# Performance work log

Hardware: AMD Instinct MI355X
Metric: run time of the kernel (lower is better)

The kernel has to match this reference:

```python
import jax, jax.numpy as jnp
import numpy as np

KERNELS = (4, 4, 8, 8, 8, 16, 16)
HEADS = (4, 4, 8, 8, 8, 16, 16)
PATCH = 2
EPS = 1e-5


def _layer_norm(x, w, b):
    mu = jnp.mean(x, axis=-1, keepdims=True)
    var = jnp.mean(jnp.square(x - mu), axis=-1, keepdims=True)
    return (x - mu) * jax.lax.rsqrt(var + EPS) * w + b


def _sliding_kernel_attention(x, w_qkv, k, heads):
    # x: (B, H, W, C) channels-last. Unfold -> per-window attention over the
    # k*k pixels (token dim = C) -> overlap-add fold (stride 1).
    B, H, W, C = x.shape
    Lh, Lw = H - k + 1, W - k + 1
    scale = (C // heads) ** -0.5
    ih = jnp.arange(Lh)[:, None] + jnp.arange(k)[None, :]   # (Lh, k)
    iw = jnp.arange(Lw)[:, None] + jnp.arange(k)[None, :]   # (Lw, k)
    pat = x[:, ih][:, :, :, iw]                             # (B, Lh, k, Lw, k, C)
    tok = pat.transpose(0, 1, 3, 2, 4, 5).reshape(B, Lh * Lw, k * k, C)
    qkv = jnp.einsum('blnc,dc->blnd', tok, w_qkv)           # (B, L, k*k, 3C)
    q, kk, v = jnp.split(qkv, 3, axis=-1)
    attn = jax.nn.softmax(jnp.einsum('blqc,blkc->blqk', q, kk) * scale, axis=-1)
    o = jnp.einsum('blqk,blkc->blqc', attn, v)              # (B, L, k*k, C)
    o = o.reshape(B, Lh, Lw, k, k, C).transpose(0, 1, 3, 2, 4, 5)  # (B,Lh,k,Lw,k,C)
    # overlap-add fold back to (B, H, W, C); duplicate indices accumulate
    return jnp.zeros_like(x).at[:, ih[:, :, None, None], iw[None, None, :, :], :].add(o)


def _block(x, ln1_w, ln1_b, w_qkv, ln2_w, ln2_b, w1, b1, w2, b2, k, heads):
    x = x + _sliding_kernel_attention(_layer_norm(x, ln1_w, ln1_b), w_qkv, k, heads)
    h = _layer_norm(x, ln2_w, ln2_b)
    h = jax.nn.gelu(h @ w1.T + b1, approximate=False)
    return x + (h @ w2.T + b2)


def _forward(x, patch_w, patch_b, row_emb, col_emb, cls_tok, ln1_w, ln1_b, qkv_w,
             ln2_w, ln2_b, mlp_w1, mlp_b1, mlp_w2, mlp_b2, cls_w, cls_b):
    # patch embed: conv k=stride=PATCH; output laid out channels-last (B, G, G, C)
    h = jax.lax.conv_general_dilated(
        x, patch_w, (PATCH, PATCH), 'VALID',
        dimension_numbers=('NCHW', 'OIHW', 'NHWC')) + patch_b
    B, G, _, C = h.shape
    # 2D positional embedding: row half + col half concatenated on channels
    pos = jnp.concatenate([
        jnp.broadcast_to(row_emb[:, None, :], (G, G, C // 2)),
        jnp.broadcast_to(col_emb[None, :, :], (G, G, C // 2))], axis=-1)
    h = h + pos
    # cls token: one extra row prepended along H (torch cat on dim=2)
    cls = jnp.broadcast_to(cls_tok, (B, 1, G, C))
    h = jnp.concatenate([cls, h], axis=1)                   # (B, G+1, G, C)
    for i in range(7):
        h = _block(h, ln1_w[i], ln1_b[i], qkv_w[i], ln2_w[i], ln2_b[i],
                   mlp_w1[i], mlp_b1[i], mlp_w2[i], mlp_b2[i],
                   KERNELS[i], HEADS[i])
    return h[:, 0, 0, :] @ cls_w.T + cls_b                  # (B, num_classes)


def setup_inputs() -> dict:
    key = jax.random.key(0)
    ks = jax.random.split(key, 8)
    B, C, G, NCLS, NB = 16, 256, 16, 1000, 7
    s = 0.02
    return {
        'x': jax.random.normal(ks[0], (B, 3, 32, 32), jnp.float32),
        'patch_w': jax.random.normal(ks[1], (C, 3, PATCH, PATCH), jnp.float32) * s,
        'patch_b': jnp.zeros((C,), jnp.float32),
        'row_emb': jax.random.normal(ks[2], (G, C // 2), jnp.float32) * s,
        'col_emb': jax.random.normal(ks[3], (G, C // 2), jnp.float32) * s,
        'cls_tok': jnp.zeros((C,), jnp.float32),
        'ln1_w': jnp.ones((NB, C), jnp.float32),
        'ln1_b': jnp.zeros((NB, C), jnp.float32),
        'qkv_w': jax.random.normal(ks[4], (NB, 3 * C, C), jnp.float32) * s,
        'ln2_w': jnp.ones((NB, C), jnp.float32),
        'ln2_b': jnp.zeros((NB, C), jnp.float32),
        'mlp_w1': jax.random.normal(ks[5], (NB, 2 * C, C), jnp.float32) * s,
        'mlp_b1': jnp.zeros((NB, 2 * C), jnp.float32),
        'mlp_w2': jax.random.normal(ks[6], (NB, C, 2 * C), jnp.float32) * s,
        'mlp_b2': jnp.zeros((NB, C), jnp.float32),
        'cls_w': jax.random.normal(ks[7], (NCLS, C), jnp.float32) * s,
        'cls_b': jnp.zeros((NCLS,), jnp.float32),
    }


def reference(x, patch_w, patch_b, row_emb, col_emb, cls_tok, ln1_w, ln1_b, qkv_w,
              ln2_w, ln2_b, mlp_w1, mlp_b1, mlp_w2, mlp_b2, cls_w, cls_b):
    return _forward(x, patch_w, patch_b, row_emb, col_emb, cls_tok, ln1_w, ln1_b,
                    qkv_w, ln2_w, ln2_b, mlp_w1, mlp_b1, mlp_w2, mlp_b2, cls_w, cls_b)
```

## Files before the change

kernel.cpp:

```cpp
#include <hip/hip_runtime.h>
#include <cmath>

#define NPIX 4352
#define C_DIM 256

typedef unsigned short ushort_t;
typedef unsigned int uint_t;
typedef float f32x4 __attribute__((ext_vector_type(4)));
typedef __bf16 bfx8 __attribute__((ext_vector_type(8)));

__device__ __forceinline__ ushort_t f2bf(float f) {
    uint_t u = __float_as_uint(f);
    u = (u + 0x7FFFu + ((u >> 16) & 1u)) >> 16;
    return (ushort_t)u;
}
__device__ __forceinline__ float bf2f(ushort_t b) {
    return __uint_as_float(((uint_t)b) << 16);
}
__device__ __forceinline__ float gelu_f(float v) {
    return 0.5f * v * (1.0f + erff(v * 0.70710678118654752f));
}

__global__ __launch_bounds__(256) void conv3_bf16(
    const float* __restrict__ a, ushort_t* __restrict__ oa, int na,
    const float* __restrict__ b, ushort_t* __restrict__ ob, int nb,
    const float* __restrict__ c, ushort_t* __restrict__ oc, int nc)
{
    int ntot = na + nb + nc;
    for (int i = blockIdx.x * 256 + threadIdx.x; i < ntot; i += gridDim.x * 256) {
        if (i < na)            oa[i] = f2bf(a[i]);
        else if (i < na + nb)  ob[i - na] = f2bf(b[i - na]);
        else                   oc[i - na - nb] = f2bf(c[i - na - nb]);
    }
}

__global__ __launch_bounds__(256) void patch_embed_ln(
    const float* __restrict__ x, const float* __restrict__ pw,
    const float* __restrict__ pb, const float* __restrict__ row_emb,
    const float* __restrict__ col_emb, const float* __restrict__ cls_tok,
    const float* __restrict__ lw, const float* __restrict__ lb,
    float* __restrict__ out, ushort_t* __restrict__ lnout)
{
    __shared__ float red[8];
    int p = blockIdx.x;
    int c = threadIdx.x;
    int b = p / 272;
    int rem = p - b * 272;
    int y = rem >> 4;
    int xw = rem & 15;
    float v;
    if (y == 0) {
        v = cls_tok[c];
    } else {
        int gr = y - 1, gc = xw;
        const float* xb = x + (size_t)b * 3 * 1024;
        const float* wc = pw + (size_t)c * 12;
        float acc = pb[c];
        #pragma unroll
        for (int ci = 0; ci < 3; ci++)
            #pragma unroll
            for (int ph = 0; ph < 2; ph++)
                #pragma unroll
                for (int pq = 0; pq < 2; pq++)
                    acc += xb[ci * 1024 + (2 * gr + ph) * 32 + (2 * gc + pq)]
                         * wc[(ci * 2 + ph) * 2 + pq];
        acc += (c < 128) ? row_emb[gr * 128 + c] : col_emb[gc * 128 + (c - 128)];
        v = acc;
    }
    out[(size_t)p * C_DIM + c] = v;
    float s = v;
    s += __shfl_down(s, 32); s += __shfl_down(s, 16); s += __shfl_down(s, 8);
    s += __shfl_down(s, 4);  s += __shfl_down(s, 2);  s += __shfl_down(s, 1);
    if ((c & 63) == 0) red[c >> 6] = s;
    __syncthreads();
    float mu = (red[0] + red[1] + red[2] + red[3]) * (1.0f / 256.0f);
    float d = v - mu;
    float s2 = d * d;
    s2 += __shfl_down(s2, 32); s2 += __shfl_down(s2, 16); s2 += __shfl_down(s2, 8);
    s2 += __shfl_down(s2, 4);  s2 += __shfl_down(s2, 2);  s2 += __shfl_down(s2, 1);
    if ((c & 63) == 0) red[4 + (c >> 6)] = s2;
    __syncthreads();
    float var = (red[4] + red[5] + red[6] + red[7]) * (1.0f / 256.0f);
    lnout[(size_t)p * C_DIM + c] = f2bf(d * rsqrtf(var + 1e-5f) * lw[c] + lb[c]);
}

__global__ __launch_bounds__(256) void layernorm_k(
    const float* __restrict__ in, const float* __restrict__ w,
    const float* __restrict__ b, ushort_t* __restrict__ out)
{
    __shared__ float red[8];
    int r = blockIdx.x, c = threadIdx.x;
    float v = in[(size_t)r * C_DIM + c];
    float s = v;
    s += __shfl_down(s, 32); s += __shfl_down(s, 16); s += __shfl_down(s, 8);
    s += __shfl_down(s, 4);  s += __shfl_down(s, 2);  s += __shfl_down(s, 1);
    if ((c & 63) == 0) red[c >> 6] = s;
    __syncthreads();
    float mu = (red[0] + red[1] + red[2] + red[3]) * (1.0f / 256.0f);
    float d = v - mu;
    float s2 = d * d;
    s2 += __shfl_down(s2, 32); s2 += __shfl_down(s2, 16); s2 += __shfl_down(s2, 8);
    s2 += __shfl_down(s2, 4);  s2 += __shfl_down(s2, 2);  s2 += __shfl_down(s2, 1);
    if ((c & 63) == 0) red[4 + (c >> 6)] = s2;
    __syncthreads();
    float var = (red[4] + red[5] + red[6] + red[7]) * (1.0f / 256.0f);
    out[(size_t)r * C_DIM + c] = f2bf(d * rsqrtf(var + 1e-5f) * w[c] + b[c]);
}

template <int BM, int BN, int MODE>
__global__ __launch_bounds__(256) void gemm_v2(
    const ushort_t* __restrict__ A, const ushort_t* __restrict__ B,
    const float* __restrict__ bias, const float* __restrict__ res,
    void* __restrict__ outp, ushort_t* __restrict__ vT, int K, int ldo)
{
    constexpr int MI = BM / 32, NJ = BN / 32;
    constexpr int AG = BM * 4, BG = BN * 4;
    constexpr int AU = AG / 256, BU = BG / 256;
    constexpr int HALF = (BM + BN) * 32;
    constexpr int STAGE_E = 2 * HALF;
    constexpr int BOUNCE_E = BM * (BN + 8);
    constexpr int SMEM_E = (STAGE_E > BOUNCE_E) ? STAGE_E : BOUNCE_E;
    __shared__ ushort_t sm[SMEM_E];

    int m0 = blockIdx.x * BM, n0 = blockIdx.y * BN;
    int t = threadIdx.x, lane = t & 63, wv = t >> 6;
    int l15 = lane & 15, lg = lane >> 4;
    int wr = wv >> 1, wc = wv & 1;

    const int nt = K / 32;
    f32x4 acc[MI][NJ] = {};
    uint4 ra[AU], rb[BU];

    #pragma unroll
    for (int u = 0; u < AU; u++) {
        int g = t + u * 256, row = g >> 2, p = g & 3;
        int ps = p ^ ((row >> 1) & 3);
        ra[u] = *(const uint4*)(A + (size_t)(m0 + row) * K + ps * 8);
    }
    #pragma unroll
    for (int u = 0; u < BU; u++) {
        int g = t + u * 256, col = g >> 2, p = g & 3;
        int ps = p ^ ((col >> 1) & 3);
        rb[u] = *(const uint4*)(B + (size_t)(n0 + col) * K + ps * 8);
    }
    #pragma unroll
    for (int u = 0; u < AU; u++) *(uint4*)(sm + (t + u * 256) * 8) = ra[u];
    #pragma unroll
    for (int u = 0; u < BU; u++) *(uint4*)(sm + BM * 32 + (t + u * 256) * 8) = rb[u];
    __syncthreads();

    for (int ks = 0; ks < nt; ks++) {
        int coff = (ks & 1) * HALF, noff = ((ks & 1) ^ 1) * HALF;
        if (ks + 1 < nt) {
            int k1 = (ks + 1) * 32;
            #pragma unroll
            for (int u = 0; u < AU; u++) {
                int g = t + u * 256, row = g >> 2, p = g & 3;
                int ps = p ^ ((row >> 1) & 3);
                ra[u] = *(const uint4*)(A + (size_t)(m0 + row) * K + k1 + ps * 8);
            }
            #pragma unroll
            for (int u = 0; u < BU; u++) {
                int g = t + u * 256, col = g >> 2, p = g & 3;
                int ps = p ^ ((col >> 1) & 3);
                rb[u] = *(const uint4*)(B + (size_t)(n0 + col) * K + k1 + ps * 8);
            }
        }
        bfx8 af[MI], bf[NJ];
        #pragma unroll
        for (int i = 0; i < MI; i++) {
            int row = wr * (BM / 2) + i * 16 + l15;
            af[i] = *(const bfx8*)(sm + coff + row * 32 + ((lg ^ ((row >> 1) & 3)) << 3));
        }
        #pragma unroll
        for (int j = 0; j < NJ; j++) {
            int col = wc * (BN / 2) + j * 16 + l15;
            bf[j] = *(const bfx8*)(sm + coff + BM * 32 + col * 32 + ((lg ^ ((col >> 1) & 3)) << 3));
        }
        #pragma unroll
        for (int i = 0; i < MI; i++)
            #pragma unroll
            for (int j = 0; j < NJ; j++)
                acc[i][j] = __builtin_amdgcn_mfma_f32_16x16x32_bf16(af[i], bf[j], acc[i][j], 0, 0, 0);
        if (ks + 1 < nt) {
            #pragma unroll
            for (int u = 0; u < AU; u++) *(uint4*)(sm + noff + (t + u * 256) * 8) = ra[u];
            #pragma unroll
            for (int u = 0; u < BU; u++) *(uint4*)(sm + noff + BM * 32 + (t + u * 256) * 8) = rb[u];
        }
        __syncthreads();
    }

    if (MODE == 0 && n0 >= 512) {
        #pragma unroll
        for (int i = 0; i < MI; i++) {
            int mb = m0 + wr * (BM / 2) + i * 16 + lg * 4;
            #pragma unroll
            for (int j = 0; j < NJ; j++) {
                int nv = n0 - 512 + wc * (BN / 2) + j * 16 + l15;
                ushort4 pk;
                pk.x = f2bf(acc[i][j][0]); pk.y = f2bf(acc[i][j][1]);
                pk.z = f2bf(acc[i][j][2]); pk.w = f2bf(acc[i][j][3]);
                *(ushort4*)&vT[(size_t)nv * NPIX + mb] = pk;
            }
        }
        return;
    }
    if (MODE == 3) {
        float* o = (float*)outp;
        #pragma unroll
        for (int i = 0; i < MI; i++) {
            #pragma unroll
            for (int j = 0; j < NJ; j++) {
                int col = n0 + wc * (BN / 2) + j * 16 + l15;
                float bz = bias[col];
                #pragma unroll
                for (int r = 0; r < 4; r++) {
                    int row = m0 + wr * (BM / 2) + i * 16 + lg * 4 + r;
                    o[(size_t)row * ldo + col] = acc[i][j][r] + bz + res[(size_t)row * ldo + col];
                }
            }
        }
        return;
    }
    __syncthreads();
    #pragma unroll
    for (int i = 0; i < MI; i++) {
        #pragma unroll
        for (int j = 0; j < NJ; j++) {
            int cl = wc * (BN / 2) + j * 16 + l15;
            float bz = (MODE == 2) ? bias[n0 + cl] : 0.0f;
            #pragma unroll
            for (int r = 0; r < 4; r++) {
                int rl = wr * (BM / 2) + i * 16 + lg * 4 + r;
                float v = acc[i][j][r];
                if (MODE == 2) v = gelu_f(v + bz);
                sm[rl * (BN + 8) + cl] = f2bf(v);
            }
        }
    }
    __syncthreads();
    ushort_t* ob = (ushort_t*)outp;
    #pragma unroll
    for (int e = 0; e < BM * BN; e += 2048) {
        int idx = e + t * 8;
        int rl = idx / BN, cl = idx % BN;
        uint4 v = *(const uint4*)(sm + rl * (BN + 8) + cl);
        *(uint4*)&ob[(size_t)(m0 + rl) * ldo + n0 + cl] = v;
    }
}

__device__ __forceinline__ uint2 ld_u4_align(const uint_t* drow, int e0) {
    int d0 = e0 >> 1;
    if (!(e0 & 1)) return make_uint2(drow[d0], drow[d0 + 1]);
    uint_t a = drow[d0], b = drow[d0 + 1], c = drow[d0 + 2];
    return make_uint2((a >> 16) | (b << 16), (b >> 16) | (c << 16));
}
__device__ __forceinline__ uint4 ld_u8_align(const uint_t* drow, int e0) {
    int d0 = e0 >> 1;
    if (!(e0 & 1)) return make_uint4(drow[d0], drow[d0 + 1], drow[d0 + 2], drow[d0 + 3]);
    uint_t a = drow[d0], b = drow[d0 + 1], c = drow[d0 + 2], d = drow[d0 + 3], e = drow[d0 + 4];
    return make_uint4((a >> 16) | (b << 16), (b >> 16) | (c << 16),
                      (c >> 16) | (d << 16), (d >> 16) | (e << 16));
}

template <int KK>
__global__ __launch_bounds__(256) void attn_v2(
    const ushort_t* __restrict__ qk, const ushort_t* __restrict__ vT,
    ushort_t* __restrict__ obuf, int w0, int nW, float scale)
{
    constexpr int T = KK * KK;
    constexpr int Lh = 18 - KK, Lw = 17 - KK, L = Lh * Lw;
    constexpr int NCH  = (KK == 16) ? 4 : 1;
    constexpr int NF   = (KK == 4) ? 1 : 4;
    constexpr int NJ   = 8;
    constexpr int PSTR = (KK == 4) ? 40 : 72;
    constexpr int KROWS = (KK == 4) ? 32 : 64;
    constexpr int VROWS = (KK == 4) ? 256 : 128;
    constexpr int PVKT = (KK == 4) ? 1 : 2;
    constexpr int EOFF = (KK == 4) ? 2048 : 4096;
    constexpr int ESTR = (KK == 4) ? 128 : 134;

    __shared__ ushort_t Klds[KROWS * 256];
    __shared__ ushort_t Vlds[VROWS * 64];
    __shared__ ushort_t Plds[4][16 * PSTR];

    int t = threadIdx.x, lane = t & 63, wv = t >> 6;
    int l15 = lane & 15, lg = lane >> 4;

    int wrel, qbase, chalf, wloc;
    if (KK == 4)      { wrel = blockIdx.x * 2 + (wv & 1); wloc = wv & 1; chalf = wv >> 1; qbase = 0; }
    else if (KK == 8) { wrel = blockIdx.x >> 1; wloc = 0; chalf = blockIdx.x & 1; qbase = wv * 16; }
    else              { wrel = blockIdx.x >> 3; wloc = 0; chalf = blockIdx.x & 1;
                        qbase = ((blockIdx.x >> 1) & 3) * 64 + wv * 16; }
    if (wrel >= nW) wrel = nW - 1;

    int pbs[2];
    #pragma unroll
    for (int w = 0; w < 2; w++) {
        int wi = (KK == 4) ? blockIdx.x * 2 + w : wrel;
        if (wi >= nW) wi = nW - 1;
        wi += w0;
        int b = wi / L, lrem = wi % L;
        pbs[w] = b * 272 + (lrem / Lw) * 16 + (lrem % Lw);
    }

    int qtok = qbase + l15;
    int qpix;
    if (KK == 4)      qpix = pbs[wloc] + ((qtok >> 2) << 4) + (qtok & 3);
    else if (KK == 8) qpix = pbs[0] + ((qtok >> 3) << 4) + (qtok & 7);
    else              qpix = pbs[0] + qtok;
    bfx8 qf[8];
    #pragma unroll
    for (int cs = 0; cs < 8; cs++)
        qf[cs] = *(const bfx8*)(qk + (size_t)qpix * 512 + cs * 32 + lg * 8);

    f32x4 o[NJ] = {};
    float mold[4] = {-1e30f, -1e30f, -1e30f, -1e30f};
    float lsum[4] = {0.f, 0.f, 0.f, 0.f};

    for (int ch = 0; ch < NCH; ch++) {
        int c0 = ch * 64;
        if (ch > 0) __syncthreads();
        for (int g = t; g < KROWS * 32; g += 256) {
            int row = g >> 5, cg = g & 31;
            int pix;
            if (KK == 4)      pix = pbs[row >> 4] + (((row & 15) >> 2) << 4) + (row & 3);
            else if (KK == 8) pix = pbs[0] + ((row >> 3) << 4) + (row & 7);
            else              pix = pbs[0] + c0 + row;
            uint4 v = *(const uint4*)(qk + (size_t)pix * 512 + 256 + cg * 8);
            *(uint4*)(Klds + row * 256 + ((cg ^ (row & 7)) << 3)) = v;
        }
        for (int g = t; g < VROWS * 8; g += 256) {
            int cr = g >> 3, c16 = g & 7;
            int cglob = (KK == 4) ? cr : chalf * 128 + cr;
            const uint_t* drow = (const uint_t*)(vT + (size_t)cglob * NPIX);
            uint4 v;
            if (KK == 4) {
                int w = c16 >> 2, sub = c16 & 3;
                if (sub < 2) {
                    int pix0 = pbs[w] + (sub << 5);
                    uint2 a  = ld_u4_align(drow, pix0);
                    uint2 b2 = ld_u4_align(drow, pix0 + 16);
                    v = make_uint4(a.x, a.y, b2.x, b2.y);
                } else v = make_uint4(0, 0, 0, 0);
            } else if (KK == 8) {
                v = ld_u8_align(drow, pbs[0] + (c16 << 4));
            } else {
                v = *(const uint4*)(vT + (size_t)cglob * NPIX + pbs[0] + c0 + (c16 << 3));
            }
            *(uint4*)(Vlds + cr * 64 + ((c16 ^ (cr & 7)) << 3)) = v;
        }
        __syncthreads();
        f32x4 s[NF];
        #pragma unroll
        for (int j = 0; j < NF; j++) s[j] = f32x4{0.f, 0.f, 0.f, 0.f};
        #pragma unroll
        for (int cs = 0; cs < 8; cs++) {
            #pragma unroll
            for (int j = 0; j < NF; j++) {
                int krow = (KK == 4) ? (wloc << 4) + l15 : (j << 4) + l15;
                bfx8 kf = *(const bfx8*)(Klds + krow * 256 + ((((cs << 2) + lg) ^ (krow & 7)) << 3));
                s[j] = __builtin_amdgcn_mfma_f32_16x16x32_bf16(qf[cs], kf, s[j], 0, 0, 0);
            }
        }
        float alpha[4];
        float p[NF][4];
        #pragma unroll
        for (int r = 0; r < 4; r++) {
            float mx = s[0][r];
            #pragma unroll
            for (int j = 1; j < NF; j++) mx = fmaxf(mx, s[j][r]);
            mx = fmaxf(mx, __shfl_xor(mx, 1));
            mx = fmaxf(mx, __shfl_xor(mx, 2));
            mx = fmaxf(mx, __shfl_xor(mx, 4));
            mx = fmaxf(mx, __shfl_xor(mx, 8));
            float mnew = fmaxf(mold[r], mx);
            alpha[r] = __expf(scale * (mold[r] - mnew));
            float ps = 0.f;
            #pragma unroll
            for (int j = 0; j < NF; j++) {
                p[j][r] = __expf(scale * (s[j][r] - mnew));
                ps += p[j][r];
            }
            ps += __shfl_xor(ps, 1);
            ps += __shfl_xor(ps, 2);
            ps += __shfl_xor(ps, 4);
            ps += __shfl_xor(ps, 8);
            lsum[r] = lsum[r] * alpha[r] + ps;
            mold[r] = mnew;
        }
        if (NCH > 1) {
            #pragma unroll
            for (int j = 0; j < NJ; j++) {
                o[j][0] *= alpha[0]; o[j][1] *= alpha[1];
                o[j][2] *= alpha[2]; o[j][3] *= alpha[3];
            }
        }
        ushort_t* Pw = Plds[wv];
        #pragma unroll
        for (int j = 0; j < NF; j++)
            #pragma unroll
            for (int r = 0; r < 4; r++)
                Pw[(lg * 4 + r) * PSTR + (j << 4) + l15] = f2bf(p[j][r]);
        if (KK == 4) {
            #pragma unroll
            for (int r = 0; r < 4; r++)
                Pw[(lg * 4 + r) * PSTR + 16 + l15] = 0;
        }
        asm volatile("s_waitcnt lgkmcnt(0)" ::: "memory");
        __builtin_amdgcn_sched_barrier(0);
        #pragma unroll
        for (int kt = 0; kt < PVKT; kt++) {
            bfx8 pf = *(const bfx8*)(Pw + l15 * PSTR + (kt << 5) + (lg << 3));
            #pragma unroll
            for (int j = 0; j < NJ; j++) {
                int cr = (KK == 4) ? chalf * 128 + (j << 4) + l15 : (j << 4) + l15;
                int c16 = ((KK == 4) ? (wloc << 2) + lg : (kt << 2) + lg) ^ (cr & 7);
                bfx8 vf = *(const bfx8*)(Vlds + cr * 64 + (c16 << 3));
                o[j] = __builtin_amdgcn_mfma_f32_16x16x32_bf16(pf, vf, o[j], 0, 0, 0);
            }
        }
    }
    asm volatile("s_waitcnt lgkmcnt(0)" ::: "memory");
    __syncthreads();
    float inv[4];
    #pragma unroll
    for (int r = 0; r < 4; r++) inv[r] = 1.0f / lsum[r];
    ushort_t* Ep = Klds + wv * EOFF;
    #pragma unroll
    for (int j = 0; j < NJ; j++)
        #pragma unroll
        for (int r = 0; r < 4; r++)
            Ep[(lg * 4 + r) * ESTR + (j << 4) + l15] = f2bf(o[j][r] * inv[r]);
    asm volatile("s_waitcnt lgkmcnt(0)" ::: "memory");
    __builtin_amdgcn_sched_barrier(0);
    size_t gb = ((size_t)wrel * T + qbase) * C_DIM + chalf * 128;
    #pragma unroll
    for (int i = 0; i < 4; i++) {
        int off = i * 512 + lane * 8;
        int row = off >> 7, col = off & 127;
        uint4 v = *(const uint4*)(Ep + row * ESTR + col);
        *(uint4*)(obuf + gb + (size_t)row * C_DIM + col) = v;
    }
}

__global__ __launch_bounds__(256) void fold_ln(
    const ushort_t* __restrict__ obuf, const float* __restrict__ xin,
    float* __restrict__ y, const float* __restrict__ lw,
    const float* __restrict__ lb, ushort_t* __restrict__ lnout, int do_ln,
    int k, int Lh, int Lw, int w0, int w1)
{
    __shared__ float red[8];
    int p = blockIdx.x;
    int c = threadIdx.x;
    int b = p / 272;
    int rem = p - b * 272;
    int yy = rem >> 4, xx = rem & 15;
    int L = Lh * Lw;
    int T = k * k;
    float acc = xin ? xin[(size_t)p * C_DIM + c] : y[(size_t)p * C_DIM + c];
    int lh0 = max(0, yy - k + 1), lh1 = min(Lh - 1, yy);
    int lw0 = max(0, xx - k + 1), lw1 = min(Lw - 1, xx);
    for (int lh = lh0; lh <= lh1; lh++) {
        for (int lw = lw0; lw <= lw1; lw++) {
            int widx = b * L + lh * Lw + lw;
            if (widx < w0 || widx >= w1) continue;
            int n = (yy - lh) * k + (xx - lw);
            acc += bf2f(obuf[((size_t)(widx - w0) * T + n) * C_DIM + c]);
        }
    }
    y[(size_t)p * C_DIM + c] = acc;
    if (!do_ln) return;
    float s = acc;
    s += __shfl_down(s, 32); s += __shfl_down(s, 16); s += __shfl_down(s, 8);
    s += __shfl_down(s, 4);  s += __shfl_down(s, 2);  s += __shfl_down(s, 1);
    if ((c & 63) == 0) red[c >> 6] = s;
    __syncthreads();
    float mu = (red[0] + red[1] + red[2] + red[3]) * (1.0f / 256.0f);
    float d = acc - mu;
    float s2 = d * d;
    s2 += __shfl_down(s2, 32); s2 += __shfl_down(s2, 16); s2 += __shfl_down(s2, 8);
    s2 += __shfl_down(s2, 4);  s2 += __shfl_down(s2, 2);  s2 += __shfl_down(s2, 1);
    if ((c & 63) == 0) red[4 + (c >> 6)] = s2;
    __syncthreads();
    float var = (red[4] + red[5] + red[6] + red[7]) * (1.0f / 256.0f);
    lnout[(size_t)p * C_DIM + c] = f2bf(d * rsqrtf(var + 1e-5f) * lw[c] + lb[c]);
}

__global__ __launch_bounds__(256) void classifier_k(
    const float* __restrict__ h, const float* __restrict__ cw,
    const float* __restrict__ cb, float* __restrict__ out)
{
    __shared__ float hrow[256];
    int b = blockIdx.x;
    int n = blockIdx.y * 256 + threadIdx.x;
    hrow[threadIdx.x] = h[(size_t)b * 272 * C_DIM + threadIdx.x];
    __syncthreads();
    if (n < 1000) {
        float acc = cb[n];
        const float* wr = cw + (size_t)n * C_DIM;
        for (int c = 0; c < 256; c++) acc += hrow[c] * wr[c];
        out[(size_t)b * 1000 + n] = acc;
    }
}

extern "C" void kernel_launch(void* const* d_in, const int* in_sizes, int n_in,
                              void* d_out, int out_size, void* d_ws, size_t ws_size,
                              hipStream_t stream)
{
    const float* x       = (const float*)d_in[0];
    const float* patch_w = (const float*)d_in[1];
    const float* patch_b = (const float*)d_in[2];
    const float* row_emb = (const float*)d_in[3];
    const float* col_emb = (const float*)d_in[4];
    const float* cls_tok = (const float*)d_in[5];
    const float* ln1_w   = (const float*)d_in[6];
    const float* ln1_b   = (const float*)d_in[7];
    const float* qkv_w   = (const float*)d_in[8];
    const float* ln2_w   = (const float*)d_in[9];
    const float* ln2_b   = (const float*)d_in[10];
    const float* mlp_w1  = (const float*)d_in[11];
    const float* mlp_b1  = (const float*)d_in[12];
    const float* mlp_w2  = (const float*)d_in[13];
    const float* mlp_b2  = (const float*)d_in[14];
    const float* cls_w   = (const float*)d_in[15];
    const float* cls_b   = (const float*)d_in[16];
    float* out = (float*)d_out;

    float* xb0  = (float*)d_ws;
    float* xb1  = xb0 + (size_t)NPIX * 256;
    ushort_t* lnb = (ushort_t*)(xb1 + (size_t)NPIX * 256);
    ushort_t* qkb = lnb + (size_t)NPIX * 256;
    ushort_t* vT  = qkb + (size_t)NPIX * 512;
    ushort_t* h1  = vT + (size_t)256 * NPIX;
    ushort_t* wq  = h1 + (size_t)NPIX * 512;
    ushort_t* w1b = wq + (size_t)7 * 768 * 256;
    ushort_t* w2b = w1b + (size_t)7 * 512 * 256;
    ushort_t* obuf = w2b + (size_t)7 * 256 * 512;
    size_t obuf_off_bytes = (size_t)((char*)obuf - (char*)d_ws);
    size_t obuf_cap_e = (ws_size > obuf_off_bytes + 64)
                        ? (ws_size - obuf_off_bytes - 64) / 2 : 0;

    conv3_bf16<<<1024, 256, 0, stream>>>(qkv_w, wq, 7 * 768 * 256,
                                         mlp_w1, w1b, 7 * 512 * 256,
                                         mlp_w2, w2b, 7 * 256 * 512);

    patch_embed_ln<<<NPIX, 256, 0, stream>>>(x, patch_w, patch_b, row_emb,
                                             col_emb, cls_tok, ln1_w, ln1_b,
                                             xb0, lnb);

    const int KS[7] = {4, 4, 8, 8, 8, 16, 16};
    float* xcur = xb0;
    float* ybuf = xb1;

    for (int i = 0; i < 7; i++) {
        int k = KS[i];
        int Lh = 18 - k, Lw = 17 - k, L = Lh * Lw, T = k * k;
        float scale = 1.0f / std::sqrt((float)(256 / k));

        if (i > 0)
            layernorm_k<<<NPIX, 256, 0, stream>>>(xcur, ln1_w + i * 256,
                                                  ln1_b + i * 256, lnb);
        gemm_v2<128, 128, 0><<<dim3(NPIX / 128, 6), 256, 0, stream>>>(
            lnb, wq + (size_t)i * 768 * 256, nullptr, nullptr, qkb, vT, 256, 512);

        int totalW = 16 * L;
        size_t perW = (size_t)T * C_DIM;
        int maxW = (int)((obuf_cap_e / perW) < (size_t)totalW
                         ? (obuf_cap_e / perW) : (size_t)totalW);
        if (maxW < 2) maxW = 2;
        if (k == 4) maxW &= ~1;
        for (int w0 = 0; w0 < totalW; w0 += maxW) {
            int nW = totalW - w0 < maxW ? totalW - w0 : maxW;
            if (k == 4)
                attn_v2<4><<<(nW + 1) / 2, 256, 0, stream>>>(qkb, vT, obuf, w0, nW, scale);
            else if (k == 8)
                attn_v2<8><<<nW * 2, 256, 0, stream>>>(qkb, vT, obuf, w0, nW, scale);
            else
                attn_v2<16><<<nW * 8, 256, 0, stream>>>(qkb, vT, obuf, w0, nW, scale);
            int last = (w0 + nW >= totalW);
            fold_ln<<<NPIX, 256, 0, stream>>>(obuf, (w0 == 0) ? xcur : nullptr,
                                              ybuf, ln2_w + i * 256, ln2_b + i * 256,
                                              lnb, last, k, Lh, Lw, w0, w0 + nW);
        }

        gemm_v2<64, 128, 2><<<dim3(NPIX / 64, 4), 256, 0, stream>>>(
            lnb, w1b + (size_t)i * 512 * 256, mlp_b1 + i * 512, nullptr, h1, nullptr, 256, 512);
        gemm_v2<64, 64, 3><<<dim3(NPIX / 64, 4), 256, 0, stream>>>(
            h1, w2b + (size_t)i * 256 * 512, mlp_b2 + i * 256, ybuf, xcur, nullptr, 512, 256);
    }

    classifier_k<<<dim3(16, 4), 256, 0, stream>>>(xcur, cls_w, cls_b, out);
}
```

Baseline: 763.3 us.

## Add full-window k=8 attention kernel and GEMM-based path for k=16

The k=8 layers get a dedicated attention kernel where one block covers a whole window and all 256 channels, so K and V are staged once instead of split across two channel-half blocks. For k=16, each sequence has only 2x1 windows, so attention becomes three kernels: a batched QK^T GEMM writing fp32 scores, a row softmax, and a PV GEMM. This replaces the chunked online-softmax kernel that launched 8 blocks per window. attn_v2 is reduced to a k=4-only specialization. The cost is extra global round trips for the score and probability buffers and more kernel launches.

```diff
diff --git a/kernel.cpp b/kernel.cpp
--- a/kernel.cpp
+++ b/kernel.cpp
@@ -271,15 +271,13 @@
 {
     constexpr int T = KK * KK;
     constexpr int Lh = 18 - KK, Lw = 17 - KK, L = Lh * Lw;
-    constexpr int NCH  = (KK == 16) ? 4 : 1;
-    constexpr int NF   = (KK == 4) ? 1 : 4;
+    constexpr int NF   = 1;
     constexpr int NJ   = 8;
-    constexpr int PSTR = (KK == 4) ? 40 : 72;
-    constexpr int KROWS = (KK == 4) ? 32 : 64;
-    constexpr int VROWS = (KK == 4) ? 256 : 128;
-    constexpr int PVKT = (KK == 4) ? 1 : 2;
-    constexpr int EOFF = (KK == 4) ? 2048 : 4096;
-    constexpr int ESTR = (KK == 4) ? 128 : 134;
+    constexpr int PSTR = 40;
+    constexpr int KROWS = 32;
+    constexpr int VROWS = 256;
+    constexpr int EOFF = 2048;
+    constexpr int ESTR = 128;
 
     __shared__ ushort_t Klds[KROWS * 256];
     __shared__ ushort_t Vlds[VROWS * 64];
@@ -288,17 +286,14 @@
     int t = threadIdx.x, lane = t & 63, wv = t >> 6;
     int l15 = lane & 15, lg = lane >> 4;
 
-    int wrel, qbase, chalf, wloc;
-    if (KK == 4)      { wrel = blockIdx.x * 2 + (wv & 1); wloc = wv & 1; chalf = wv >> 1; qbase = 0; }
-    else if (KK == 8) { wrel = blockIdx.x >> 1; wloc = 0; chalf = blockIdx.x & 1; qbase = wv * 16; }
-    else              { wrel = blockIdx.x >> 3; wloc = 0; chalf = blockIdx.x & 1;
-                        qbase = ((blockIdx.x >> 1) & 3) * 64 + wv * 16; }
+    int wrel = blockIdx.x * 2 + (wv & 1);
+    int wloc = wv & 1, chalf = wv >> 1, qbase = 0;
     if (wrel >= nW) wrel = nW - 1;
 
     int pbs[2];
     #pragma unroll
     for (int w = 0; w < 2; w++) {
-        int wi = (KK == 4) ? blockIdx.x * 2 + w : wrel;
+        int wi = blockIdx.x * 2 + w;
         if (wi >= nW) wi = nW - 1;
         wi += w0;
         int b = wi / L, lrem = wi % L;
@@ -306,120 +301,77 @@
     }
 
     int qtok = qbase + l15;
-    int qpix;
-    if (KK == 4)      qpix = pbs[wloc] + ((qtok >> 2) << 4) + (qtok & 3);
-    else if (KK == 8) qpix = pbs[0] + ((qtok >> 3) << 4) + (qtok & 7);
-    else              qpix = pbs[0] + qtok;
+    int qpix = pbs[wloc] + ((qtok >> 2) << 4) + (qtok & 3);
     bfx8 qf[8];
     #pragma unroll
     for (int cs = 0; cs < 8; cs++)
         qf[cs] = *(const bfx8*)(qk + (size_t)qpix * 512 + cs * 32 + lg * 8);
 
     f32x4 o[NJ] = {};
-    float mold[4] = {-1e30f, -1e30f, -1e30f, -1e30f};
     float lsum[4] = {0.f, 0.f, 0.f, 0.f};
 
-    for (int ch = 0; ch < NCH; ch++) {
-        int c0 = ch * 64;
-        if (ch > 0) __syncthreads();
-        for (int g = t; g < KROWS * 32; g += 256) {
-            int row = g >> 5, cg = g & 31;
-            int pix;
-            if (KK == 4)      pix = pbs[row >> 4] + (((row & 15) >> 2) << 4) + (row & 3);
-            else if (KK == 8) pix = pbs[0] + ((row >> 3) << 4) + (row & 7);
-            else              pix = pbs[0] + c0 + row;
-            uint4 v = *(const uint4*)(qk + (size_t)pix * 512 + 256 + cg * 8);
-            *(uint4*)(Klds + row * 256 + ((cg ^ (row & 7)) << 3)) = v;
-        }
-        for (int g = t; g < VROWS * 8; g += 256) {
-            int cr = g >> 3, c16 = g & 7;
-            int cglob = (KK == 4) ? cr : chalf * 128 + cr;
-            const uint_t* drow = (const uint_t*)(vT + (size_t)cglob * NPIX);
-            uint4 v;
-            if (KK == 4) {
-                int w = c16 >> 2, sub = c16 & 3;
-                if (sub < 2) {
-                    int pix0 = pbs[w] + (sub << 5);
-                    uint2 a  = ld_u4_align(drow, pix0);
-                    uint2 b2 = ld_u4_align(drow, pix0 + 16);
-                    v = make_uint4(a.x, a.y, b2.x, b2.y);
-                } else v = make_uint4(0, 0, 0, 0);
-            } else if (KK == 8) {
-                v = ld_u8_align(drow, pbs[0] + (c16 << 4));
-            } else {
-                v = *(const uint4*)(vT + (size_t)cglob * NPIX + pbs[0] + c0 + (c16 << 3));
-            }
-            *(uint4*)(Vlds + cr * 64 + ((c16 ^ (cr & 7)) << 3)) = v;
-        }
-        __syncthreads();
-        f32x4 s[NF];
-        #pragma unroll
-        for (int j = 0; j < NF; j++) s[j] = f32x4{0.f, 0.f, 0.f, 0.f};
-        #pragma unroll
-        for (int cs = 0; cs < 8; cs++) {
-            #pragma unroll
-            for (int j = 0; j < NF; j++) {
-                int krow = (KK == 4) ? (wloc << 4) + l15 : (j << 4) + l15;
-                bfx8 kf = *(const bfx8*)(Klds + krow * 256 + ((((cs << 2) + lg) ^ (krow & 7)) << 3));
-                s[j] = __builtin_amdgcn_mfma_f32_16x16x32_bf16(qf[cs], kf, s[j], 0, 0, 0);
-            }
-        }
-        float alpha[4];
-        float p[NF][4];
-        #pragma unroll
-        for (int r = 0; r < 4; r++) {
-            float mx = s[0][r];
-            #pragma unroll
-            for (int j = 1; j < NF; j++) mx = fmaxf(mx, s[j][r]);
-            mx = fmaxf(mx, __shfl_xor(mx, 1));
-            mx = fmaxf(mx, __shfl_xor(mx, 2));
-            mx = fmaxf(mx, __shfl_xor(mx, 4));
-            mx = fmaxf(mx, __shfl_xor(mx, 8));
-            float mnew = fmaxf(mold[r], mx);
-            alpha[r] = __expf(scale * (mold[r] - mnew));
-            float ps = 0.f;
-            #pragma unroll
-            for (int j = 0; j < NF; j++) {
-                p[j][r] = __expf(scale * (s[j][r] - mnew));
-                ps += p[j][r];
-            }
-            ps += __shfl_xor(ps, 1);
-            ps += __shfl_xor(ps, 2);
-            ps += __shfl_xor(ps, 4);
-            ps += __shfl_xor(ps, 8);
-            lsum[r] = lsum[r] * alpha[r] + ps;
-            mold[r] = mnew;
-        }
-        if (NCH > 1) {
-            #pragma unroll
-            for (int j = 0; j < NJ; j++) {
-                o[j][0] *= alpha[0]; o[j][1] *= alpha[1];
-                o[j][2] *= alpha[2]; o[j][3] *= alpha[3];
-            }
-        }
-        ushort_t* Pw = Plds[wv];
-        #pragma unroll
-        for (int j = 0; j < NF; j++)
-            #pragma unroll
-            for (int r = 0; r < 4; r++)
-                Pw[(lg * 4 + r) * PSTR + (j << 4) + l15] = f2bf(p[j][r]);
-        if (KK == 4) {
-            #pragma unroll
-            for (int r = 0; r < 4; r++)
-                Pw[(lg * 4 + r) * PSTR + 16 + l15] = 0;
-        }
-        asm volatile("s_waitcnt lgkmcnt(0)" ::: "memory");
-        __builtin_amdgcn_sched_barrier(0);
-        #pragma unroll
-        for (int kt = 0; kt < PVKT; kt++) {
-            bfx8 pf = *(const bfx8*)(Pw + l15 * PSTR + (kt << 5) + (lg << 3));
-            #pragma unroll
-            for (int j = 0; j < NJ; j++) {
-                int cr = (KK == 4) ? chalf * 128 + (j << 4) + l15 : (j << 4) + l15;
-                int c16 = ((KK == 4) ? (wloc << 2) + lg : (kt << 2) + lg) ^ (cr & 7);
-                bfx8 vf = *(const bfx8*)(Vlds + cr * 64 + (c16 << 3));
-                o[j] = __builtin_amdgcn_mfma_f32_16x16x32_bf16(pf, vf, o[j], 0, 0, 0);
-            }
+    for (int g = t; g < KROWS * 32; g += 256) {
+        int row = g >> 5, cg = g & 31;
+        int pix = pbs[row >> 4] + (((row & 15) >> 2) << 4) + (row & 3);
+        uint4 v = *(const uint4*)(qk + (size_t)pix * 512 + 256 + cg * 8);
+        *(uint4*)(Klds + row * 256 + ((cg ^ (row & 7)) << 3)) = v;
+    }
+    for (int g = t; g < VROWS * 8; g += 256) {
+        int cr = g >> 3, c16 = g & 7;
+        const uint_t* drow = (const uint_t*)(vT + (size_t)cr * NPIX);
+        uint4 v;
+        int w = c16 >> 2, sub = c16 & 3;
+        if (sub < 2) {
+            int pix0 = pbs[w] + (sub << 5);
+            uint2 a  = ld_u4_align(drow, pix0);
+            uint2 b2 = ld_u4_align(drow, pix0 + 16);
+            v = make_uint4(a.x, a.y, b2.x, b2.y);
+        } else v = make_uint4(0, 0, 0, 0);
+        *(uint4*)(Vlds + cr * 64 + ((c16 ^ (cr & 7)) << 3)) = v;
+    }
+    __syncthreads();
+    f32x4 s[NF];
+    #pragma unroll
+    for (int j = 0; j < NF; j++) s[j] = f32x4{0.f, 0.f, 0.f, 0.f};
+    #pragma unroll
+    for (int cs = 0; cs < 8; cs++) {
+        int krow = (wloc << 4) + l15;
+        bfx8 kf = *(const bfx8*)(Klds + krow * 256 + ((((cs << 2) + lg) ^ (krow & 7)) << 3));
+        s[0] = __builtin_amdgcn_mfma_f32_16x16x32_bf16(qf[cs], kf, s[0], 0, 0, 0);
+    }
+    float p[NF][4];
+    #pragma unroll
+    for (int r = 0; r < 4; r++) {
+        float mx = s[0][r];
+        mx = fmaxf(mx, __shfl_xor(mx, 1));
+        mx = fmaxf(mx, __shfl_xor(mx, 2));
+        mx = fmaxf(mx, __shfl_xor(mx, 4));
+        mx = fmaxf(mx, __shfl_xor(mx, 8));
+        float ps = 0.f;
+        p[0][r] = __expf(scale * (s[0][r] - mx));
+        ps += p[0][r];
+        ps += __shfl_xor(ps, 1);
+        ps += __shfl_xor(ps, 2);
+        ps += __shfl_xor(ps, 4);
+        ps += __shfl_xor(ps, 8);
+        lsum[r] = ps;
+    }
+    ushort_t* Pw = Plds[wv];
+    #pragma unroll
+    for (int r = 0; r < 4; r++) {
+        Pw[(lg * 4 + r) * PSTR + l15] = f2bf(p[0][r]);
+        Pw[(lg * 4 + r) * PSTR + 16 + l15] = 0;
+    }
+    asm volatile("s_waitcnt lgkmcnt(0)" ::: "memory");
+    __builtin_amdgcn_sched_barrier(0);
+    {
+        bfx8 pf = *(const bfx8*)(Pw + l15 * PSTR + (lg << 3));
+        #pragma unroll
+        for (int j = 0; j < NJ; j++) {
+            int cr = chalf * 128 + (j << 4) + l15;
+            int c16 = ((wloc << 2) + lg) ^ (cr & 7);
+            bfx8 vf = *(const bfx8*)(Vlds + cr * 64 + (c16 << 3));
+            o[j] = __builtin_amdgcn_mfma_f32_16x16x32_bf16(pf, vf, o[j], 0, 0, 0);
         }
     }
     asm volatile("s_waitcnt lgkmcnt(0)" ::: "memory");
@@ -443,6 +395,249 @@
         uint4 v = *(const uint4*)(Ep + row * ESTR + col);
         *(uint4*)(obuf + gb + (size_t)row * C_DIM + col) = v;
     }
+}
+
+__global__ __launch_bounds__(256) void attn_v3(
+    const ushort_t* __restrict__ qk, const ushort_t* __restrict__ vT,
+    ushort_t* __restrict__ obuf, int w0, float scale)
+{
+    __shared__ ushort_t SH[32768];
+    const int Lw = 9, L = 90;
+    int t = threadIdx.x, lane = t & 63, wv = t >> 6;
+    int l15 = lane & 15, lg = lane >> 4;
+    int wrel = blockIdx.x;
+    int widx = w0 + wrel;
+    int b = widx / L, lrem = widx % L;
+    int pbase = b * 272 + (lrem / Lw) * 16 + (lrem % Lw);
+    int qbase = wv * 16;
+
+    int qtok = qbase + l15;
+    int qpix = pbase + ((qtok >> 3) << 4) + (qtok & 7);
+    bfx8 qf[8];
+    #pragma unroll
+    for (int cs = 0; cs < 8; cs++)
+        qf[cs] = *(const bfx8*)(qk + (size_t)qpix * 512 + cs * 32 + lg * 8);
+
+    for (int g = t; g < 64 * 32; g += 256) {
+        int row = g >> 5, cg = g & 31;
+        int pix = pbase + ((row >> 3) << 4) + (row & 7);
+        uint4 v = *(const uint4*)(qk + (size_t)pix * 512 + 256 + cg * 8);
+        *(uint4*)(SH + row * 256 + ((cg ^ (row & 7)) << 3)) = v;
+    }
+    for (int g = t; g < 256 * 8; g += 256) {
+        int cr = g >> 3, c16 = g & 7;
+        const uint_t* drow = (const uint_t*)(vT + (size_t)cr * NPIX);
+        uint4 v = ld_u8_align(drow, pbase + (c16 << 4));
+        *(uint4*)(SH + 16384 + cr * 64 + ((c16 ^ (cr & 7)) << 3)) = v;
+    }
+    __syncthreads();
+
+    f32x4 s[4];
+    #pragma unroll
+    for (int j = 0; j < 4; j++) s[j] = f32x4{0.f, 0.f, 0.f, 0.f};
+    #pragma unroll
+    for (int cs = 0; cs < 8; cs++) {
+        #pragma unroll
+        for (int j = 0; j < 4; j++) {
+            int krow = (j << 4) + l15;
+            bfx8 kf = *(const bfx8*)(SH + krow * 256 + ((((cs << 2) + lg) ^ (krow & 7)) << 3));
+            s[j] = __builtin_amdgcn_mfma_f32_16x16x32_bf16(qf[cs], kf, s[j], 0, 0, 0);
+        }
+    }
+    float p[4][4], lsum[4];
+    #pragma unroll
+    for (int r = 0; r < 4; r++) {
+        float mx = s[0][r];
+        #pragma unroll
+        for (int j = 1; j < 4; j++) mx = fmaxf(mx, s[j][r]);
+        mx = fmaxf(mx, __shfl_xor(mx, 1));
+        mx = fmaxf(mx, __shfl_xor(mx, 2));
+        mx = fmaxf(mx, __shfl_xor(mx, 4));
+        mx = fmaxf(mx, __shfl_xor(mx, 8));
+        float ps = 0.f;
+        #pragma unroll
+        for (int j = 0; j < 4; j++) {
+            p[j][r] = __expf(scale * (s[j][r] - mx));
+            ps += p[j][r];
+        }
+        ps += __shfl_xor(ps, 1);
+        ps += __shfl_xor(ps, 2);
+        ps += __shfl_xor(ps, 4);
+        ps += __shfl_xor(ps, 8);
+        lsum[r] = ps;
+    }
+    __syncthreads();
+    ushort_t* Pw = SH + wv * 1088;
+    #pragma unroll
+    for (int j = 0; j < 4; j++)
+        #pragma unroll
+        for (int r = 0; r < 4; r++)
+            Pw[(lg * 4 + r) * 68 + (j << 4) + l15] = f2bf(p[j][r]);
+    asm volatile("s_waitcnt lgkmcnt(0)" ::: "memory");
+    __builtin_amdgcn_sched_barrier(0);
+    f32x4 o[16] = {};
+    #pragma unroll
+    for (int kt = 0; kt < 2; kt++) {
+        bfx8 pf = *(const bfx8*)(Pw + l15 * 68 + (kt << 5) + (lg << 3));
+        #pragma unroll
+        for (int j = 0; j < 16; j++) {
+            int cr = (j << 4) + l15;
+            int c16 = ((kt << 2) + lg) ^ (cr & 7);
+            bfx8 vf = *(const bfx8*)(SH + 16384 + cr * 64 + (c16 << 3));
+            o[j] = __builtin_amdgcn_mfma_f32_16x16x32_bf16(pf, vf, o[j], 0, 0, 0);
+        }
+    }
+    asm volatile("s_waitcnt lgkmcnt(0)" ::: "memory");
+    __syncthreads();
+    float inv[4];
+    #pragma unroll
+    for (int r = 0; r < 4; r++) inv[r] = 1.0f / lsum[r];
+    ushort_t* Ep = SH + wv * 4224;
+    #pragma unroll
+    for (int j = 0; j < 16; j++)
+        #pragma unroll
+        for (int r = 0; r < 4; r++)
+            Ep[(lg * 4 + r) * 260 + (j << 4) + l15] = f2bf(o[j][r] * inv[r]);
+    asm volatile("s_waitcnt lgkmcnt(0)" ::: "memory");
+    __builtin_amdgcn_sched_barrier(0);
+    size_t gb = ((size_t)wrel * 64 + qbase) * C_DIM;
+    #pragma unroll
+    for (int i = 0; i < 8; i++) {
+        int off = i * 512 + lane * 8;
+        int row = off >> 8, col = off & 255;
+        uint4 v = *(const uint4*)(Ep + row * 260 + col);
+        *(uint4*)(obuf + gb + off) = v;
+    }
+}
+
+template <int PASS>
+__global__ __launch_bounds__(256) void gemm_seq(
+    const ushort_t* __restrict__ A, const ushort_t* __restrict__ B,
+    const float* __restrict__ linv, void* __restrict__ outp)
+{
+    __shared__ ushort_t sm[8192];
+    int m0 = blockIdx.x * 64, n0 = blockIdx.y * 64;
+    int seq = blockIdx.z;
+    int pbase = (seq >> 1) * 272 + (seq & 1) * 16;
+    int t = threadIdx.x, lane = t & 63, wv = t >> 6;
+    int l15 = lane & 15, lg = lane >> 4;
+    int wr = wv >> 1, wc = wv & 1;
+
+    f32x4 acc[2][2] = {};
+    uint4 ra, rb;
+
+    int g_row = t >> 2, g_p = t & 3;
+    int g_ps = g_p ^ ((g_row >> 1) & 3);
+
+    const ushort_t* Asrc;
+    const ushort_t* Bsrc;
+    if (PASS == 0) {
+        Asrc = A + (size_t)(pbase + m0 + g_row) * 512 + g_ps * 8;
+        Bsrc = B + (size_t)(pbase + n0 + g_row) * 512 + 256 + g_ps * 8;
+    } else {
+        Asrc = A + (size_t)seq * 65536 + (size_t)(m0 + g_row) * 256 + g_ps * 8;
+        Bsrc = B + (size_t)(n0 + g_row) * NPIX + pbase + g_ps * 8;
+    }
+
+    ra = *(const uint4*)(Asrc);
+    rb = *(const uint4*)(Bsrc);
+    *(uint4*)(sm + t * 8) = ra;
+    *(uint4*)(sm + 2048 + t * 8) = rb;
+    __syncthreads();
+
+    for (int ks = 0; ks < 8; ks++) {
+        int coff = (ks & 1) * 4096, noff = ((ks & 1) ^ 1) * 4096;
+        if (ks + 1 < 8) {
+            int k1 = (ks + 1) * 32;
+            ra = *(const uint4*)(Asrc + k1);
+            rb = *(const uint4*)(Bsrc + k1);
+        }
+        bfx8 af[2], bf[2];
+        #pragma unroll
+        for (int i = 0; i < 2; i++) {
+            int row = wr * 32 + i * 16 + l15;
+            af[i] = *(const bfx8*)(sm + coff + row * 32 + ((lg ^ ((row >> 1) & 3)) << 3));
+        }
+        #pragma unroll
+        for (int j = 0; j < 2; j++) {
+            int col = wc * 32 + j * 16 + l15;
+            bf[j] = *(const bfx8*)(sm + coff + 2048 + col * 32 + ((lg ^ ((col >> 1) & 3)) << 3));
+        }
+        #pragma unroll
+        for (int i = 0; i < 2; i++)
+            #pragma unroll
+            for (int j = 0; j < 2; j++)
+                acc[i][j] = __builtin_amdgcn_mfma_f32_16x16x32_bf16(af[i], bf[j], acc[i][j], 0, 0, 0);
+        if (ks + 1 < 8) {
+            *(uint4*)(sm + noff + t * 8) = ra;
+            *(uint4*)(sm + noff + 2048 + t * 8) = rb;
+        }
+        __syncthreads();
+    }
+
+    if (PASS == 0) {
+        float* S = (float*)outp + (size_t)seq * 65536;
+        #pragma unroll
+        for (int i = 0; i < 2; i++) {
+            #pragma unroll
+            for (int j = 0; j < 2; j++) {
+                int col = n0 + wc * 32 + j * 16 + l15;
+                #pragma unroll
+                for (int r = 0; r < 4; r++) {
+                    int row = m0 + wr * 32 + i * 16 + lg * 4 + r;
+                    S[(size_t)row * 256 + col] = acc[i][j][r];
+                }
+            }
+        }
+        return;
+    }
+    ushort_t* ob = (ushort_t*)outp;
+    #pragma unroll
+    for (int i = 0; i < 2; i++) {
+        #pragma unroll
+        for (int j = 0; j < 2; j++) {
+            int cl = wc * 32 + j * 16 + l15;
+            #pragma unroll
+            for (int r = 0; r < 4; r++) {
+                int rl = wr * 32 + i * 16 + lg * 4 + r;
+                float v = acc[i][j][r] * linv[seq * 256 + m0 + rl];
+                sm[rl * 72 + cl] = f2bf(v);
+            }
+        }
+    }
+    __syncthreads();
+    #pragma unroll
+    for (int e = 0; e < 4096; e += 2048) {
+        int idx = e + t * 8;
+        int rl = idx >> 6, cl = idx & 63;
+        uint4 v = *(const uint4*)(sm + rl * 72 + cl);
+        *(uint4*)&ob[(size_t)seq * 65536 + (size_t)(m0 + rl) * 256 + n0 + cl] = v;
+    }
+}
+
+__global__ __launch_bounds__(256) void rowsm(
+    const float* __restrict__ sbuf, ushort_t* __restrict__ pbuf,
+    float* __restrict__ linv, float scale)
+{
+    __shared__ float red[8];
+    int r = blockIdx.x, t = threadIdx.x;
+    float s = sbuf[(size_t)r * 256 + t];
+    float m = s;
+    m = fmaxf(m, __shfl_down(m, 32)); m = fmaxf(m, __shfl_down(m, 16));
+    m = fmaxf(m, __shfl_down(m, 8));  m = fmaxf(m, __shfl_down(m, 4));
+    m = fmaxf(m, __shfl_down(m, 2));  m = fmaxf(m, __shfl_down(m, 1));
+    if ((t & 63) == 0) red[t >> 6] = m;
+    __syncthreads();
+    m = fmaxf(fmaxf(red[0], red[1]), fmaxf(red[2], red[3]));
+    float p = __expf(scale * (s - m));
+    float ps = p;
+    ps += __shfl_down(ps, 32); ps += __shfl_down(ps, 16); ps += __shfl_down(ps, 8);
+    ps += __shfl_down(ps, 4);  ps += __shfl_down(ps, 2);  ps += __shfl_down(ps, 1);
+    if ((t & 63) == 0) red[4 + (t >> 6)] = ps;
+    __syncthreads();
+    float sum = red[4] + red[5] + red[6] + red[7];
+    pbuf[(size_t)r * 256 + t] = f2bf(p);
+    if (t == 0) linv[r] = 1.0f / sum;
 }
 
 __global__ __launch_bounds__(256) void fold_ln(
@@ -537,7 +732,10 @@
     ushort_t* wq  = h1 + (size_t)NPIX * 512;
     ushort_t* w1b = wq + (size_t)7 * 768 * 256;
     ushort_t* w2b = w1b + (size_t)7 * 512 * 256;
-    ushort_t* obuf = w2b + (size_t)7 * 256 * 512;
+    float* sbuf   = (float*)(w2b + (size_t)7 * 256 * 512);
+    ushort_t* pbuf = (ushort_t*)(sbuf + (size_t)32 * 65536);
+    float* linv   = (float*)(pbuf + (size_t)32 * 65536);
+    ushort_t* obuf = (ushort_t*)(linv + 8192);
     size_t obuf_off_bytes = (size_t)((char*)obuf - (char*)d_ws);
     size_t obuf_cap_e = (ws_size > obuf_off_bytes + 64)
                         ? (ws_size - obuf_off_bytes - 64) / 2 : 0;
@@ -565,24 +763,31 @@
         gemm_v2<128, 128, 0><<<dim3(NPIX / 128, 6), 256, 0, stream>>>(
             lnb, wq + (size_t)i * 768 * 256, nullptr, nullptr, qkb, vT, 256, 512);
 
-        int totalW = 16 * L;
-        size_t perW = (size_t)T * C_DIM;
-        int maxW = (int)((obuf_cap_e / perW) < (size_t)totalW
-                         ? (obuf_cap_e / perW) : (size_t)totalW);
-        if (maxW < 2) maxW = 2;
-        if (k == 4) maxW &= ~1;
-        for (int w0 = 0; w0 < totalW; w0 += maxW) {
-            int nW = totalW - w0 < maxW ? totalW - w0 : maxW;
-            if (k == 4)
-                attn_v2<4><<<(nW + 1) / 2, 256, 0, stream>>>(qkb, vT, obuf, w0, nW, scale);
-            else if (k == 8)
-                attn_v2<8><<<nW * 2, 256, 0, stream>>>(qkb, vT, obuf, w0, nW, scale);
-            else
-                attn_v2<16><<<nW * 8, 256, 0, stream>>>(qkb, vT, obuf, w0, nW, scale);
-            int last = (w0 + nW >= totalW);
-            fold_ln<<<NPIX, 256, 0, stream>>>(obuf, (w0 == 0) ? xcur : nullptr,
-                                              ybuf, ln2_w + i * 256, ln2_b + i * 256,
-                                              lnb, last, k, Lh, Lw, w0, w0 + nW);
+        if (k == 16) {
+            gemm_seq<0><<<dim3(4, 4, 32), 256, 0, stream>>>(qkb, qkb, nullptr, sbuf);
+            rowsm<<<8192, 256, 0, stream>>>(sbuf, pbuf, linv, scale);
+            gemm_seq<1><<<dim3(4, 4, 32), 256, 0, stream>>>(pbuf, vT, linv, obuf);
+            fold_ln<<<NPIX, 256, 0, stream>>>(obuf, xcur, ybuf,
+                                              ln2_w + i * 256, ln2_b + i * 256,
+                                              lnb, 1, k, Lh, Lw, 0, 32);
+        } else {
+            int totalW = 16 * L;
+            size_t perW = (size_t)T * C_DIM;
+            int maxW = (int)((obuf_cap_e / perW) < (size_t)totalW
+                             ? (obuf_cap_e / perW) : (size_t)totalW);
+            if (maxW < 2) maxW = 2;
+            if (k == 4) maxW &= ~1;
+            for (int w0 = 0; w0 < totalW; w0 += maxW) {
+                int nW = totalW - w0 < maxW ? totalW - w0 : maxW;
+                if (k == 4)
+                    attn_v2<4><<<(nW + 1) / 2, 256, 0, stream>>>(qkb, vT, obuf, w0, nW, scale);
+                else
+                    attn_v3<<<nW, 256, 0, stream>>>(qkb, vT, obuf, w0, scale);
+                int last = (w0 + nW >= totalW);
+                fold_ln<<<NPIX, 256, 0, stream>>>(obuf, (w0 == 0) ? xcur : nullptr,
+                                                  ybuf, ln2_w + i * 256, ln2_b + i * 256,
+                                                  lnb, last, k, Lh, Lw, w0, w0 + nW);
+            }
         }
 
         gemm_v2<64, 128, 2><<<dim3(NPIX / 64, 4), 256, 0, stream>>>(
```

Result: faster. 725.6 us (-4.9%).
